# Optimization experiments

Hardware: AMD Instinct MI355X
Metric: run time of the kernel (lower is better)

## Reference

```python
import jax, jax.numpy as jnp
import numpy as np

B, H, P, D = 4, 16, 1024, 128

def setup_inputs() -> dict:
    key = jax.random.key(0)
    kq, kk = jax.random.split(key)
    q = jax.random.normal(kq, (B, H, P, D), dtype=jnp.float32)
    k = jax.random.normal(kk, (B, H, P, D), dtype=jnp.float32)
    scale = jnp.full((1,), 1.0 / np.sqrt(D), dtype=jnp.float32)
    return {"q": q, "k": k, "scale": scale}

def reference(q, k, scale):
    # base_fun (SiLU) applied as the basis nonlinearity on q and k,
    # then patch-wise attention scores scaled by `scale`, softmax over keys.
    qb = jax.nn.silu(q)  # [B,H,P,D]
    kb = jax.nn.silu(k)  # [B,H,P,D]
    scores = jnp.einsum('bhpd,bhqd->bhpq', qb, kb) * scale  # [B,H,P,P]
    return jax.nn.softmax(scores, axis=-1)
```

## Files before the change

kernel.cpp:

```cpp
#include <hip/hip_runtime.h>
#include <stdint.h>
#include <stddef.h>

#define BHC 64
#define PP  1024
#define DD  128
#define BM  64
#define BN  128
#define NCH 8
#define LSTR 136

typedef __bf16 bf16x8 __attribute__((ext_vector_type(8)));
typedef float  f32x4  __attribute__((ext_vector_type(4)));

__device__ __forceinline__ unsigned short f2bf(float x) {
    union { float f; uint32_t u; } v; v.f = x;
    uint32_t r = v.u + 0x7FFFu + ((v.u >> 16) & 1u);
    return (unsigned short)(r >> 16);
}

__global__ void silu_cast_kernel(const float* __restrict__ q, const float* __restrict__ k,
                                 unsigned short* __restrict__ qb, unsigned short* __restrict__ kb,
                                 int n4each) {
    int stride = gridDim.x * blockDim.x;
    int total  = 2 * n4each;
    for (int i = blockIdx.x * blockDim.x + threadIdx.x; i < total; i += stride) {
        const float4* s; ushort4* d; int j;
        if (i < n4each) { s = (const float4*)q; d = (ushort4*)qb; j = i; }
        else            { s = (const float4*)k; d = (ushort4*)kb; j = i - n4each; }
        float4 x = s[j];
        float4 y;
        y.x = x.x / (1.f + __expf(-x.x));
        y.y = x.y / (1.f + __expf(-x.y));
        y.z = x.z / (1.f + __expf(-x.z));
        y.w = x.w / (1.f + __expf(-x.w));
        ushort4 o;
        o.x = f2bf(y.x); o.y = f2bf(y.y); o.z = f2bf(y.z); o.w = f2bf(y.w);
        d[j] = o;
    }
}

__global__ __launch_bounds__(1024) void attn_kernel(
        const unsigned short* __restrict__ qb, const unsigned short* __restrict__ kb,
        const float* __restrict__ scale, float* __restrict__ out) {
    __shared__ unsigned short qs [BM * LSTR];
    __shared__ unsigned short ksm[BN * LSTR];
    __shared__ float red_m[BM * 8];
    __shared__ float red_l[BM * 8];

    int bx   = blockIdx.x;
    int xcd  = bx & 7;
    int idx  = bx >> 3;
    int bh   = xcd * 8 + (idx >> 4);
    int qblk = idx & 15;

    int t    = threadIdx.x;
    int lane = t & 63;
    int w    = t >> 6;
    int wr   = w & 1;
    int wc   = w >> 1;
    int l15  = lane & 15;
    int quad = lane >> 4;

    const unsigned short* qg = qb + (size_t)bh * (PP * DD) + (size_t)qblk * (BM * DD);
    const unsigned short* kg = kb + (size_t)bh * (PP * DD);

    {
        int row = t >> 4, u = t & 15;
        uint4 v = *(const uint4*)(qg + row * DD + u * 8);
        *(uint4*)(&qs[row * LSTR + u * 8]) = v;
    }
    __syncthreads();

    bf16x8 aF[2][4];
#pragma unroll
    for (int rt = 0; rt < 2; ++rt)
#pragma unroll
        for (int kk = 0; kk < 4; ++kk)
            aF[rt][kk] = *(const bf16x8*)(&qs[(wr * 32 + rt * 16 + l15) * LSTR + kk * 32 + quad * 8]);

    f32x4 acc[NCH][2];
#pragma unroll
    for (int c = 0; c < NCH; ++c) {
        acc[c][0] = (f32x4)0.0f;
        acc[c][1] = (f32x4)0.0f;
    }

#pragma unroll
    for (int c = 0; c < NCH; ++c) {
        __syncthreads();
        {
            int u0 = t,        r0 = u0 >> 4, c0 = u0 & 15;
            int u1 = t + 1024, r1 = u1 >> 4, c1 = u1 & 15;
            uint4 v0 = *(const uint4*)(kg + (c * BN + r0) * DD + c0 * 8);
            uint4 v1 = *(const uint4*)(kg + (c * BN + r1) * DD + c1 * 8);
            *(uint4*)(&ksm[r0 * LSTR + c0 * 8]) = v0;
            *(uint4*)(&ksm[r1 * LSTR + c1 * 8]) = v1;
        }
        __syncthreads();
#pragma unroll
        for (int kk = 0; kk < 4; ++kk) {
            bf16x8 bF = *(const bf16x8*)(&ksm[(wc * 16 + l15) * LSTR + kk * 32 + quad * 8]);
            acc[c][0] = __builtin_amdgcn_mfma_f32_16x16x32_bf16(aF[0][kk], bF, acc[c][0], 0, 0, 0);
            acc[c][1] = __builtin_amdgcn_mfma_f32_16x16x32_bf16(aF[1][kk], bF, acc[c][1], 0, 0, 0);
        }
    }

    float C2 = scale[0] * 1.44269504088896340736f;

#pragma unroll
    for (int rt = 0; rt < 2; ++rt) {
#pragma unroll
        for (int r = 0; r < 4; ++r) {
            float m = acc[0][rt][r];
#pragma unroll
            for (int c = 1; c < NCH; ++c) m = fmaxf(m, acc[c][rt][r]);
#pragma unroll
            for (int off = 1; off < 16; off <<= 1) m = fmaxf(m, __shfl_xor(m, off, 64));
            if (l15 == 0) red_m[(wr * 32 + rt * 16 + quad * 4 + r) * 8 + wc] = m;
        }
    }
    __syncthreads();

#pragma unroll
    for (int rt = 0; rt < 2; ++rt) {
#pragma unroll
        for (int r = 0; r < 4; ++r) {
            int row = wr * 32 + rt * 16 + quad * 4 + r;
            float4 p0 = *(const float4*)(&red_m[row * 8]);
            float4 p1 = *(const float4*)(&red_m[row * 8 + 4]);
            float m = fmaxf(fmaxf(fmaxf(p0.x, p0.y), fmaxf(p0.z, p0.w)),
                            fmaxf(fmaxf(p1.x, p1.y), fmaxf(p1.z, p1.w)));
            float ssum = 0.f;
#pragma unroll
            for (int c = 0; c < NCH; ++c) {
                float e = exp2f((acc[c][rt][r] - m) * C2);
                acc[c][rt][r] = e;
                ssum += e;
            }
#pragma unroll
            for (int off = 1; off < 16; off <<= 1) ssum += __shfl_xor(ssum, off, 64);
            if (l15 == 0) red_l[row * 8 + wc] = ssum;
        }
    }
    __syncthreads();

    float inv[2][4];
#pragma unroll
    for (int rt = 0; rt < 2; ++rt) {
#pragma unroll
        for (int r = 0; r < 4; ++r) {
            int row = wr * 32 + rt * 16 + quad * 4 + r;
            float4 p0 = *(const float4*)(&red_l[row * 8]);
            float4 p1 = *(const float4*)(&red_l[row * 8 + 4]);
            float l = (p0.x + p0.y) + (p0.z + p0.w) + (p1.x + p1.y) + (p1.z + p1.w);
            inv[rt][r] = 1.0f / l;
        }
    }

    float* og = out + ((size_t)bh << 20) + (size_t)(qblk * BM) * PP;
#pragma unroll
    for (int c = 0; c < NCH; ++c) {
#pragma unroll
        for (int rt = 0; rt < 2; ++rt) {
            int key = c * BN + wc * 16 + l15;
            int rb  = wr * 32 + rt * 16 + quad * 4;
#pragma unroll
            for (int r = 0; r < 4; ++r) {
                og[(size_t)(rb + r) * PP + key] = acc[c][rt][r] * inv[rt][r];
            }
        }
    }
}

extern "C" void kernel_launch(void* const* d_in, const int* in_sizes, int n_in,
                              void* d_out, int out_size, void* d_ws, size_t ws_size,
                              hipStream_t stream) {
    const float* q     = (const float*)d_in[0];
    const float* k     = (const float*)d_in[1];
    const float* scale = (const float*)d_in[2];
    float* out = (float*)d_out;

    unsigned short* qb = (unsigned short*)d_ws;
    unsigned short* kb = qb + (size_t)BHC * PP * DD;

    int n4each = (BHC * PP * DD) / 4;
    silu_cast_kernel<<<2048, 256, 0, stream>>>(q, k, qb, kb, n4each);
    attn_kernel<<<1024, 1024, 0, stream>>>(qb, kb, scale, out);
}
```

Measured before the change: 377.6 us.

## Fuse SiLU and bf16 cast into attention kernel loads

Removes the separate SiLU/cast kernel and its bf16 workspace. The attention kernel now reads fp32 q and k directly, applies SiLU and converts to bf16 while staging tiles into shared memory. Q fragments are reloaded from LDS inside the K-chunk loop instead of being kept in registers, and that loop is no longer unrolled, presumably to relieve register pressure. The cost is that SiLU is recomputed on each K tile once per query block and twice as many global bytes are read per tile. The rolled loop also indexes the accumulator array with a runtime index, which risks moving it to scratch memory.

```diff
diff --git a/kernel.cpp b/kernel.cpp
--- a/kernel.cpp
+++ b/kernel.cpp
@@ -19,29 +19,12 @@
     return (unsigned short)(r >> 16);
 }
 
-__global__ void silu_cast_kernel(const float* __restrict__ q, const float* __restrict__ k,
-                                 unsigned short* __restrict__ qb, unsigned short* __restrict__ kb,
-                                 int n4each) {
-    int stride = gridDim.x * blockDim.x;
-    int total  = 2 * n4each;
-    for (int i = blockIdx.x * blockDim.x + threadIdx.x; i < total; i += stride) {
-        const float4* s; ushort4* d; int j;
-        if (i < n4each) { s = (const float4*)q; d = (ushort4*)qb; j = i; }
-        else            { s = (const float4*)k; d = (ushort4*)kb; j = i - n4each; }
-        float4 x = s[j];
-        float4 y;
-        y.x = x.x / (1.f + __expf(-x.x));
-        y.y = x.y / (1.f + __expf(-x.y));
-        y.z = x.z / (1.f + __expf(-x.z));
-        y.w = x.w / (1.f + __expf(-x.w));
-        ushort4 o;
-        o.x = f2bf(y.x); o.y = f2bf(y.y); o.z = f2bf(y.z); o.w = f2bf(y.w);
-        d[j] = o;
-    }
+__device__ __forceinline__ float silu_f(float x) {
+    return x / (1.0f + __expf(-x));
 }
 
-__global__ __launch_bounds__(1024) void attn_kernel(
-        const unsigned short* __restrict__ qb, const unsigned short* __restrict__ kb,
+__global__ __launch_bounds__(1024) void attn_fused(
+        const float* __restrict__ q, const float* __restrict__ k,
         const float* __restrict__ scale, float* __restrict__ out) {
     __shared__ unsigned short qs [BM * LSTR];
     __shared__ unsigned short ksm[BN * LSTR];
@@ -62,22 +45,19 @@
     int l15  = lane & 15;
     int quad = lane >> 4;
 
-    const unsigned short* qg = qb + (size_t)bh * (PP * DD) + (size_t)qblk * (BM * DD);
-    const unsigned short* kg = kb + (size_t)bh * (PP * DD);
+    const float* qg = q + (size_t)bh * (PP * DD) + (size_t)qblk * (BM * DD);
+    const float* kg = k + (size_t)bh * (PP * DD);
 
-    {
-        int row = t >> 4, u = t & 15;
-        uint4 v = *(const uint4*)(qg + row * DD + u * 8);
-        *(uint4*)(&qs[row * LSTR + u * 8]) = v;
+#pragma unroll
+    for (int j = 0; j < 2; ++j) {
+        int v   = t + j * 1024;
+        int row = v >> 5, cu = v & 31;
+        float4 x = *(const float4*)(qg + row * DD + cu * 4);
+        uint2 p;
+        p.x = (uint32_t)f2bf(silu_f(x.x)) | ((uint32_t)f2bf(silu_f(x.y)) << 16);
+        p.y = (uint32_t)f2bf(silu_f(x.z)) | ((uint32_t)f2bf(silu_f(x.w)) << 16);
+        *(uint2*)(&qs[row * LSTR + cu * 4]) = p;
     }
-    __syncthreads();
-
-    bf16x8 aF[2][4];
-#pragma unroll
-    for (int rt = 0; rt < 2; ++rt)
-#pragma unroll
-        for (int kk = 0; kk < 4; ++kk)
-            aF[rt][kk] = *(const bf16x8*)(&qs[(wr * 32 + rt * 16 + l15) * LSTR + kk * 32 + quad * 8]);
 
     f32x4 acc[NCH][2];
 #pragma unroll
@@ -86,23 +66,30 @@
         acc[c][1] = (f32x4)0.0f;
     }
 
-#pragma unroll
+#pragma unroll 1
     for (int c = 0; c < NCH; ++c) {
         __syncthreads();
         {
-            int u0 = t,        r0 = u0 >> 4, c0 = u0 & 15;
-            int u1 = t + 1024, r1 = u1 >> 4, c1 = u1 & 15;
-            uint4 v0 = *(const uint4*)(kg + (c * BN + r0) * DD + c0 * 8);
-            uint4 v1 = *(const uint4*)(kg + (c * BN + r1) * DD + c1 * 8);
-            *(uint4*)(&ksm[r0 * LSTR + c0 * 8]) = v0;
-            *(uint4*)(&ksm[r1 * LSTR + c1 * 8]) = v1;
+            const float* kc = kg + c * (BN * DD);
+#pragma unroll
+            for (int j = 0; j < 4; ++j) {
+                int v   = t + j * 1024;
+                int row = v >> 5, cu = v & 31;
+                float4 x = *(const float4*)(kc + row * DD + cu * 4);
+                uint2 p;
+                p.x = (uint32_t)f2bf(silu_f(x.x)) | ((uint32_t)f2bf(silu_f(x.y)) << 16);
+                p.y = (uint32_t)f2bf(silu_f(x.z)) | ((uint32_t)f2bf(silu_f(x.w)) << 16);
+                *(uint2*)(&ksm[row * LSTR + cu * 4]) = p;
+            }
         }
         __syncthreads();
 #pragma unroll
         for (int kk = 0; kk < 4; ++kk) {
+            bf16x8 a0 = *(const bf16x8*)(&qs[(wr * 32      + l15) * LSTR + kk * 32 + quad * 8]);
+            bf16x8 a1 = *(const bf16x8*)(&qs[(wr * 32 + 16 + l15) * LSTR + kk * 32 + quad * 8]);
             bf16x8 bF = *(const bf16x8*)(&ksm[(wc * 16 + l15) * LSTR + kk * 32 + quad * 8]);
-            acc[c][0] = __builtin_amdgcn_mfma_f32_16x16x32_bf16(aF[0][kk], bF, acc[c][0], 0, 0, 0);
-            acc[c][1] = __builtin_amdgcn_mfma_f32_16x16x32_bf16(aF[1][kk], bF, acc[c][1], 0, 0, 0);
+            acc[c][0] = __builtin_amdgcn_mfma_f32_16x16x32_bf16(a0, bF, acc[c][0], 0, 0, 0);
+            acc[c][1] = __builtin_amdgcn_mfma_f32_16x16x32_bf16(a1, bF, acc[c][1], 0, 0, 0);
         }
     }
 
@@ -180,11 +167,7 @@
     const float* k     = (const float*)d_in[1];
     const float* scale = (const float*)d_in[2];
     float* out = (float*)d_out;
+    (void)d_ws; (void)ws_size; (void)in_sizes; (void)n_in; (void)out_size;
 
-    unsigned short* qb = (unsigned short*)d_ws;
-    unsigned short* kb = qb + (size_t)BHC * PP * DD;
-
-    int n4each = (BHC * PP * DD) / 4;
-    silu_cast_kernel<<<2048, 256, 0, stream>>>(q, k, qb, kb, n4each);
-    attn_kernel<<<1024, 1024, 0, stream>>>(qb, kb, scale, out);
+    attn_fused<<<1024, 1024, 0, stream>>>(q, k, scale, out);
 }
```

Result: slower. 696.6 us (+84.5%).
